# Optimization experiments

Measured on AMD Instinct MI355X. Metric: run time of the kernel, lower is better.

The kernel has to match this reference:

```python
import jax, jax.numpy as jnp
import numpy as np

B, H, W, CIN, C, L = 2, 512, 512, 64, 64, 4
TAU = 1.0


def _conv3x3(x, w):
    # NHWC input, HWIO kernel, SAME zero padding, stride 1 (SignalConv2D corr=True)
    return jax.lax.conv_general_dilated(
        x, w, window_strides=(1, 1), padding='SAME',
        dimension_numbers=('NHWC', 'HWIO', 'NHWC'))


def setup_inputs() -> dict:
    key = jax.random.key(0)
    ks = jax.random.split(key, 10)
    return {
        'x0': jax.random.normal(ks[0], (B, H, W, CIN), jnp.float32),
        'spa_mask': jax.random.uniform(ks[1], (B, H, W, 1), jnp.float32),
        'gumbel_u': jax.random.uniform(ks[2], (1, L, 2, C), jnp.float32),
        'ch_mask': jax.random.uniform(ks[3], (1, L, 2, C), jnp.float32),
        'w0': jax.random.normal(ks[4], (3, 3, CIN, C), jnp.float32) * 0.05,
        'w1': jax.random.normal(ks[5], (3, 3, C, C), jnp.float32) * 0.05,
        'w2': jax.random.normal(ks[6], (3, 3, C, C), jnp.float32) * 0.05,
        'w3': jax.random.normal(ks[7], (3, 3, C, C), jnp.float32) * 0.05,
        'w_collect': jax.random.normal(ks[8], (L * C, C), jnp.float32) * 0.05,
        'b_collect': jnp.zeros((C,), jnp.float32),
    }


def reference(x0, spa_mask, gumbel_u, ch_mask, w0, w1, w2, w3, w_collect, b_collect):
    # Gumbel-softmax channel routing mask over the {dense, sparse} axis (axis=2)
    g = -jnp.log(-jnp.log(jnp.clip(gumbel_u, 1e-10, 1.0)))
    ch = jax.nn.softmax((ch_mask + g) / TAU, axis=2)  # (1, L, 2, C)

    ws = [w0, w1, w2, w3]
    out_feats = []
    fea = x0
    for i in range(L):
        cd = ch[:, i, 0, :][:, None, None, :]  # dense-channel mask  (1,1,1,C)
        cs = ch[:, i, 1, :][:, None, None, :]  # sparse-channel mask (1,1,1,C)
        if i == 0:
            fea = _conv3x3(fea, ws[0])
            fea = fea * cs * spa_mask + fea * cd
        else:
            cdp = ch[:, i - 1, 0, :][:, None, None, :]
            csp = ch[:, i - 1, 1, :][:, None, None, :]
            fea_d = _conv3x3(fea * cdp, ws[i])
            fea_s = _conv3x3(fea * csp, ws[i])
            fea = (fea_d * cs * spa_mask + fea_d * cd
                   + fea_s * cs * spa_mask + fea_s * cd * spa_mask)
        fea = jax.nn.relu(fea)
        out_feats.append(fea)

    cat = jnp.concatenate(out_feats, axis=-1)  # (B, H, W, L*C)
    # 1x1 stride-1 Conv2DTranspose == pointwise linear + bias
    out = jnp.einsum('bhwi,io->bhwo', cat, w_collect) + b_collect
    return out, ch
```

## Files before the change

kernel.cpp:

```cpp
#include <hip/hip_runtime.h>
#include <hip/hip_fp16.h>

#define BB 2
#define HH 512
#define WW 512
#define CC 64
#define PW 514
#define PIMG (514*514)

typedef _Float16 f16;
typedef _Float16 f16x8 __attribute__((ext_vector_type(8)));
typedef _Float16 f16x4 __attribute__((ext_vector_type(4)));
typedef float f32x4 __attribute__((ext_vector_type(4)));

static __device__ __forceinline__ f16x8 zero_f16x8() {
    f16x8 z = {(f16)0,(f16)0,(f16)0,(f16)0,(f16)0,(f16)0,(f16)0,(f16)0};
    return z;
}

static __device__ __forceinline__ f16x8 cvt_pair(f32x4 a, f32x4 b) {
    f16x8 o;
    o[0]=(f16)a[0]; o[1]=(f16)a[1]; o[2]=(f16)a[2]; o[3]=(f16)a[3];
    o[4]=(f16)b[0]; o[5]=(f16)b[1]; o[6]=(f16)b[2]; o[7]=(f16)b[3];
    return o;
}

__global__ void k_prep_ch(const float* __restrict__ gum, const float* __restrict__ chm,
                          float* __restrict__ ws_ch, float* __restrict__ out_ch) {
    int t = threadIdx.x;
    int l = t >> 6, c = t & 63;
    float u0 = gum[(l*2+0)*64+c], u1 = gum[(l*2+1)*64+c];
    u0 = fminf(fmaxf(u0, 1e-10f), 1.0f);
    u1 = fminf(fmaxf(u1, 1e-10f), 1.0f);
    float a0 = chm[(l*2+0)*64+c] - logf(-logf(u0));
    float a1 = chm[(l*2+1)*64+c] - logf(-logf(u1));
    float m = fmaxf(a0, a1);
    float e0 = expf(a0-m), e1 = expf(a1-m);
    float s = e0 + e1;
    float c0 = e0/s, c1 = e1/s;
    ws_ch[(l*2+0)*64+c] = c0;  ws_ch[(l*2+1)*64+c] = c1;
    out_ch[(l*2+0)*64+c] = c0; out_ch[(l*2+1)*64+c] = c1;
}

__global__ void k_pack(const float* __restrict__ w0, const float* __restrict__ w1,
                       const float* __restrict__ w2, const float* __restrict__ w3,
                       const float* __restrict__ wc, const float* __restrict__ ch,
                       f16* __restrict__ bpk0, f16* __restrict__ bpkL, f16* __restrict__ wcpk) {
    int idx = blockIdx.x * 256 + threadIdx.x;
    if (idx < 36864) {
        int j = idx & 7, lane = (idx>>3)&63, nb = (idx>>9)&3, kb = idx>>11;
        int k = kb*32 + (lane>>4)*8 + j;
        int tap = k>>6, ci = k&63;
        int co = nb*16 + (lane&15);
        bpk0[idx] = (f16)w0[(tap*64+ci)*64+co];
    } else if (idx < 36864 + 221184) {
        int i2 = idx - 36864;
        int l = i2 / 73728;
        int r = i2 % 73728;
        int j = r&7, lane=(r>>3)&63, nb=(r>>9)&7, kb=r>>12;
        int k = kb*32 + (lane>>4)*8 + j;
        int tap = k>>6, ci = k&63;
        int copr = nb*16 + (lane&15);
        int co = copr & 63;
        const float* w = (l==0)? w1 : (l==1)? w2 : w3;
        float scale = (copr < 64) ? ch[(l*2+0)*64+ci] : ch[(l*2+1)*64+ci];
        bpkL[i2] = (f16)(w[(tap*64+ci)*64+co] * scale);
    } else if (idx < 36864 + 221184 + 16384) {
        int i3 = idx - (36864 + 221184);
        int j=i3&7, lane=(i3>>3)&63, nb=(i3>>9)&3, kb=(i3>>11)&1, l=i3>>12;
        int k = kb*32 + (lane>>4)*8 + j;
        int n = nb*16 + (lane&15);
        wcpk[i3] = (f16)wc[(l*64+k)*64+n];
    }
}

__global__ void k_guard(f16* __restrict__ buf) {
    int idx = blockIdx.x*256 + threadIdx.x;
    const int TOT = 2*2052*8;
    if (idx >= TOT) return;
    int c8 = idx & 7, g = idx >> 3;
    int b = g / 2052, r = g % 2052;
    int hp, wp;
    if      (r < 514)  { hp = 0;        wp = r; }
    else if (r < 1028) { hp = 513;      wp = r-514; }
    else if (r < 1540) { hp = r-1027;   wp = 0; }
    else               { hp = r-1539;   wp = 513; }
    *(f16x8*)(buf + ((size_t)(b*PW+hp)*PW + wp)*64 + c8*8) = zero_f16x8();
}

template<int MODE>
__global__ __launch_bounds__(256, 2) void k_conv(const void* __restrict__ in_, f16* __restrict__ out,
        const f16* __restrict__ bpk, const float* __restrict__ ch_l,
        const float* __restrict__ spa) {
    constexpr int NBT = (MODE==0) ? 4 : 8;
    constexpr int NF  = (MODE==0) ? 2 : 4;
    __shared__ f16 smem[4*136*64];
    const int wt = blockIdx.x, hb = blockIdx.y, b = blockIdx.z;
    const int h0 = hb*2;
    const int tid = threadIdx.x, lane = tid & 63, wid = tid >> 6;
    const int px0 = wt*128;
    const int sub  = lane & 7;
    const int srel = lane >> 3;
    const int cblk = sub ^ srel;

    const float* inF = (const float*)in_;

    f32x4 v0c[5], v1c[5], v0d[5], v1d[5];
    bool okc[5], okd[5];
    int dstc[5], dstd[5];

    if (MODE == 0) {
        {
            f32x4 v0[9], v1[9];
            bool ok[9];
            int dst[9];
            #pragma unroll
            for (int t = 0; t < 9; ++t) {
                int j = t*4 + wid;
                ok[t] = false;
                if (j < 34) {
                    int r = j / 17, i = j % 17;
                    int s = i*8 + srel;
                    int hin = h0 + r - 1, win = px0 + s - 1;
                    ok[t] = ((unsigned)hin < HH) && ((unsigned)win < WW);
                    dst[t] = r*17408 + i*1024 + lane*16;
                    if (ok[t]) {
                        const f32x4* p = (const f32x4*)(inF + (((size_t)(b*HH + hin)*WW + win)*CC + cblk*8));
                        v0[t] = p[0];
                        v1[t] = p[1];
                    }
                }
            }
            #pragma unroll
            for (int t = 0; t < 9; ++t) {
                if (t*4 + wid < 34) {
                    f16x8 o = ok[t] ? cvt_pair(v0[t], v1[t]) : zero_f16x8();
                    *(f16x8*)((char*)smem + dst[t]) = o;
                }
            }
        }
        __syncthreads();
        #pragma unroll
        for (int t = 0; t < 5; ++t) {
            int i = t*4 + wid;
            okc[t] = false;
            if (i < 17) {
                int s = i*8 + srel;
                int win = px0 + s - 1;
                okc[t] = (unsigned)win < WW;
                dstc[t] = 2*17408 + i*1024 + lane*16;
                if (okc[t]) {
                    const f32x4* p = (const f32x4*)(inF + (((size_t)(b*HH + h0 + 1)*WW + win)*CC + cblk*8));
                    v0c[t] = p[0];
                    v1c[t] = p[1];
                }
            }
        }
        __builtin_amdgcn_sched_barrier(0);
    } else {
        const f16* inH = (const f16*)in_;
        #pragma unroll
        for (int jj = 0; jj < 9; ++jj) {
            int j = jj*4 + wid;
            if (j < 34) {
                int r = j / 17, i = j % 17;
                int s = i*8 + srel;
                const f16* src = inH + ((size_t)(b*PW + h0 + r)*PW + (px0 + s))*64 + cblk*8;
                __builtin_amdgcn_global_load_lds(
                    (const __attribute__((address_space(1))) uint32_t*)src,
                    (__attribute__((address_space(3))) uint32_t*)
                        ((char*)smem + r*17408 + i*1024),
                    16, 0, 0);
            }
        }
        __syncthreads();
        #pragma unroll
        for (int jj = 0; jj < 9; ++jj) {
            int j = 34 + jj*4 + wid;
            if (j < 68) {
                int r = j / 17, i = j % 17;
                int s = i*8 + srel;
                const f16* src = inH + ((size_t)(b*PW + h0 + r)*PW + (px0 + s))*64 + cblk*8;
                __builtin_amdgcn_global_load_lds(
                    (const __attribute__((address_space(1))) uint32_t*)src,
                    (__attribute__((address_space(3))) uint32_t*)
                        ((char*)smem + r*17408 + i*1024),
                    16, 0, 0);
            }
        }
    }

    const int wr = wid >> 1, wn = wid & 1;
    const int lrow = lane & 15, q = lane >> 4;
    const char* smw = (const char*)smem + wr*17408;

    int sb[8][3], po[2][3];
    #pragma unroll
    for (int dxi = 0; dxi < 3; ++dxi) {
        int m7 = (lrow + dxi) & 7;
        po[0][dxi] = ((q)     ^ m7) * 16;
        po[1][dxi] = ((4 + q) ^ m7) * 16;
        #pragma unroll
        for (int mf = 0; mf < 8; ++mf)
            sb[mf][dxi] = (mf*16 + lrow + dxi) * 128;
    }

    f32x4 acc[8][NF];
    #pragma unroll
    for (int i=0;i<8;i++)
        #pragma unroll
        for (int j=0;j<NF;j++) { f32x4 z = {0.f,0.f,0.f,0.f}; acc[i][j] = z; }

    int nbIdx[4];
    nbIdx[0]=wn*2; nbIdx[1]=wn*2+1; nbIdx[2]=wn*2+4; nbIdx[3]=wn*2+5;

    const f16* blane = bpk + (size_t)lane*8;

    f16x8 acur[8], anxt[8], bcur[NF], bnxt[NF];
    #pragma unroll
    for (int nf=0; nf<NF; ++nf)
        bcur[nf] = *reinterpret_cast<const f16x8*>(blane + (size_t)nbIdx[nf]*512);
    #pragma unroll
    for (int mf=0; mf<8; ++mf)
        acur[mf] = *(const f16x8*)(smw + sb[mf][0] + po[0][0]);

    #pragma unroll
    for (int kb = 0; kb < 18; ++kb) {
        if (kb == 5) {
            if (MODE == 0) {
                #pragma unroll
                for (int t = 0; t < 5; ++t) {
                    if (t*4 + wid < 17) {
                        f16x8 o = okc[t] ? cvt_pair(v0c[t], v1c[t]) : zero_f16x8();
                        *(f16x8*)((char*)smem + dstc[t]) = o;
                    }
                }
                #pragma unroll
                for (int t = 0; t < 5; ++t) {
                    int i = t*4 + wid;
                    okd[t] = false;
                    if (i < 17) {
                        int s = i*8 + srel;
                        int hin = h0 + 2, win = px0 + s - 1;
                        okd[t] = ((unsigned)hin < HH) && ((unsigned)win < WW);
                        dstd[t] = 3*17408 + i*1024 + lane*16;
                        if (okd[t]) {
                            const f32x4* p = (const f32x4*)(inF + (((size_t)(b*HH + hin)*WW + win)*CC + cblk*8));
                            v0d[t] = p[0];
                            v1d[t] = p[1];
                        }
                    }
                }
                __builtin_amdgcn_sched_barrier(0);
            }
            __syncthreads();
        }
        if (MODE == 0 && kb == 11) {
            #pragma unroll
            for (int t = 0; t < 5; ++t) {
                if (t*4 + wid < 17) {
                    f16x8 o = okd[t] ? cvt_pair(v0d[t], v1d[t]) : zero_f16x8();
                    *(f16x8*)((char*)smem + dstd[t]) = o;
                }
            }
            __syncthreads();
        }
        if (kb < 17) {
            const int kn = kb + 1;
            const int rn = kn/6, dxin = (kn%6)/2, halfn = kn & 1;
            #pragma unroll
            for (int nf=0; nf<NF; ++nf)
                bnxt[nf] = *reinterpret_cast<const f16x8*>(blane + (size_t)(kn*NBT + nbIdx[nf])*512);
            #pragma unroll
            for (int mf=0; mf<8; ++mf)
                anxt[mf] = *(const f16x8*)(smw + rn*17408 + sb[mf][dxin] + po[halfn][dxin]);
        }
        __builtin_amdgcn_s_setprio(1);
        #pragma unroll
        for (int nf=0; nf<NF; ++nf) {
            #pragma unroll
            for (int mf=0; mf<8; ++mf)
                acc[mf][nf] = __builtin_amdgcn_mfma_f32_16x16x32_f16(acur[mf], bcur[nf], acc[mf][nf], 0,0,0);
        }
        __builtin_amdgcn_s_setprio(0);
        #pragma unroll
        for (int nf=0; nf<NF; ++nf) bcur[nf] = bnxt[nf];
        #pragma unroll
        for (int mf=0; mf<8; ++mf) acur[mf] = anxt[mf];
    }

    const float* cd = ch_l;
    const float* cs = ch_l + 64;
    const int h = h0 + wr;
    const size_t sparow = (size_t)(b*HH + h)*WW;
    const size_t outrow = (size_t)(b*PW + h + 1)*PW + 1;
    #pragma unroll
    for (int mf=0; mf<8; ++mf) {
        const int pixb = mf*16 + q*4;
        f32x4 sp4 = *(const f32x4*)(spa + sparow + px0 + pixb);
        float sp[4] = {sp4[0], sp4[1], sp4[2], sp4[3]};
        #pragma unroll
        for (int nf2=0; nf2<2; ++nf2) {
            int co = wn*32 + nf2*16 + lrow;
            float vcd = cd[co], vcs = cs[co];
            #pragma unroll
            for (int r=0; r<4; ++r) {
                float v;
                if (MODE==0) v = acc[mf][nf2][r] * (vcs*sp[r] + vcd);
                else         v = acc[mf][nf2][r] * (vcs*sp[r] + vcd) + acc[mf][nf2+2][r] * sp[r];
                v = fmaxf(v, 0.f);
                out[(outrow + px0 + pixb + r)*64 + co] = (f16)v;
            }
        }
    }
}

__global__ __launch_bounds__(256) void k_collect_all(
        const f16* __restrict__ f0, const f16* __restrict__ f1,
        const f16* __restrict__ f2, const f16* __restrict__ f3,
        const f16* __restrict__ wcpk, const float* __restrict__ bias,
        float* __restrict__ out) {
    const int wt = blockIdx.x, h = blockIdx.y, b = blockIdx.z;
    const int tid = threadIdx.x;
    const int lane = tid & 63, wid = tid >> 6;
    const int lrow = lane & 15, lk = (lane>>4)*8;
    const size_t inrow  = (size_t)(b*PW + h + 1)*PW + 1;
    const size_t outrow = (size_t)(b*HH + h)*WW;
    const int px0 = wt*256 + wid*64;

    const f16* feas[4] = {f0, f1, f2, f3};

    f32x4 acc[4][4];
    #pragma unroll
    for (int i=0;i<4;i++)
        #pragma unroll
        for (int j=0;j<4;j++) { f32x4 z = {0.f,0.f,0.f,0.f}; acc[i][j] = z; }

    f16x8 a_cur[4], a_nxt[4];
    #pragma unroll
    for (int mf=0; mf<4; ++mf)
        a_cur[mf] = *reinterpret_cast<const f16x8*>(f0 + (inrow + px0 + mf*16 + lrow)*64 + lk);

    #pragma unroll
    for (int kb=0; kb<8; ++kb) {
        if (kb < 7) {
            const f16* fl = feas[(kb+1)>>1];
            #pragma unroll
            for (int mf=0; mf<4; ++mf)
                a_nxt[mf] = *reinterpret_cast<const f16x8*>(fl + (inrow + px0 + mf*16 + lrow)*64 + ((kb+1)&1)*32 + lk);
        }
        #pragma unroll
        for (int nf=0; nf<4; ++nf) {
            f16x8 bb = *reinterpret_cast<const f16x8*>(wcpk + ((size_t)(kb*4 + nf)*64 + lane)*8);
            #pragma unroll
            for (int mf=0; mf<4; ++mf)
                acc[mf][nf] = __builtin_amdgcn_mfma_f32_16x16x32_f16(bb, a_cur[mf], acc[mf][nf], 0,0,0);
        }
        #pragma unroll
        for (int mf=0; mf<4; ++mf) a_cur[mf] = a_nxt[mf];
    }
    const int q = lane >> 4;
    #pragma unroll
    for (int mf=0; mf<4; ++mf) {
        const int pix = px0 + mf*16 + lrow;
        float* orow = out + (outrow + pix)*CC;
        #pragma unroll
        for (int nf=0; nf<4; ++nf) {
            const int co0 = nf*16 + q*4;
            f32x4 b4 = *(const f32x4*)(bias + co0);
            *(f32x4*)(orow + co0) = acc[mf][nf] + b4;
        }
    }
}

template<bool FIRST>
__global__ __launch_bounds__(256) void k_collect(const f16* __restrict__ fea,
        const f16* __restrict__ wcpk_l, const float* __restrict__ bias,
        float* __restrict__ out) {
    const int wt = blockIdx.x, h = blockIdx.y, b = blockIdx.z;
    const int tid = threadIdx.x;
    const int lane = tid & 63, wid = tid >> 6;
    const int lrow = lane & 15, lk = (lane>>4)*8;
    const size_t inrow  = (size_t)(b*PW + h + 1)*PW + 1;
    const size_t outrow = (size_t)(b*HH + h)*WW;
    const int px0 = wt*64 + wid*16;

    f32x4 acc[4];
    #pragma unroll
    for (int j=0;j<4;j++) { f32x4 z = {0.f,0.f,0.f,0.f}; acc[j] = z; }

    #pragma unroll
    for (int kb=0; kb<2; ++kb) {
        f16x8 a = *reinterpret_cast<const f16x8*>(fea + (inrow + px0 + lrow)*64 + kb*32 + lk);
        #pragma unroll
        for (int nf=0; nf<4; ++nf) {
            f16x8 bb = *reinterpret_cast<const f16x8*>(wcpk_l + ((size_t)(kb*4 + nf)*64 + lane)*8);
            acc[nf] = __builtin_amdgcn_mfma_f32_16x16x32_f16(bb, a, acc[nf], 0,0,0);
        }
    }
    const int q = lane >> 4;
    const int pix = px0 + lrow;
    float* orow = out + (outrow + pix)*CC;
    #pragma unroll
    for (int nf=0; nf<4; ++nf) {
        const int co0 = nf*16 + q*4;
        f32x4 v = acc[nf];
        #pragma unroll
        for (int r=0;r<4;++r) {
            float x = v[r];
            if (FIRST) x += bias[co0+r];
            else       x += orow[co0+r];
            orow[co0+r] = x;
        }
    }
}

extern "C" void kernel_launch(void* const* d_in, const int* in_sizes, int n_in,
                              void* d_out, int out_size, void* d_ws, size_t ws_size,
                              hipStream_t stream) {
    const float* x0  = (const float*)d_in[0];
    const float* spa = (const float*)d_in[1];
    const float* gum = (const float*)d_in[2];
    const float* chm = (const float*)d_in[3];
    const float* w0  = (const float*)d_in[4];
    const float* w1  = (const float*)d_in[5];
    const float* w2  = (const float*)d_in[6];
    const float* w3  = (const float*)d_in[7];
    const float* wc  = (const float*)d_in[8];
    const float* bias= (const float*)d_in[9];
    float* out = (float*)d_out;

    char* ws = (char*)d_ws;
    const size_t WBASE = (1u<<20);
    const size_t FB = 67699712ull;
    const size_t NEED_A = WBASE + 4*FB;
    const size_t NEED_B = WBASE + 2*FB;
    if (ws_size < NEED_B) return;

    float* ws_ch = (float*)ws;
    f16* bpk0 = (f16*)(ws + 4096);
    f16* bpkL = (f16*)(ws + 4096 + 73728);
    f16* wcpk = (f16*)(ws + 4096 + 73728 + 442368);

    k_prep_ch<<<1, 256, 0, stream>>>(gum, chm, ws_ch, out + 33554432);
    k_pack<<<1072, 256, 0, stream>>>(w0, w1, w2, w3, wc, ws_ch, bpk0, bpkL, wcpk);

    dim3 gcv(4, 256, 2);
    dim3 gca(2, 512, 2);
    dim3 gcf(8, 512, 2);

    if (ws_size >= NEED_A) {
        f16* R0 = (f16*)(ws + WBASE);
        f16* R1 = (f16*)(ws + WBASE + FB);
        f16* R2 = (f16*)(ws + WBASE + 2*FB);
        f16* R3 = (f16*)(ws + WBASE + 3*FB);
        k_guard<<<129, 256, 0, stream>>>(R1);
        k_guard<<<129, 256, 0, stream>>>(R2);
        k_guard<<<129, 256, 0, stream>>>(R3);
        k_conv<0><<<gcv, 256, 0, stream>>>(x0, R1, bpk0,          ws_ch + 0,   spa);
        k_conv<1><<<gcv, 256, 0, stream>>>(R1, R2, bpkL + 0,      ws_ch + 128, spa);
        k_conv<1><<<gcv, 256, 0, stream>>>(R2, R3, bpkL + 73728,  ws_ch + 256, spa);
        k_conv<1><<<gcv, 256, 0, stream>>>(R3, R0, bpkL + 147456, ws_ch + 384, spa);
        k_collect_all<<<gca, 256, 0, stream>>>(R1, R2, R3, R0, wcpk, bias, out);
    } else {
        f16* P0 = (f16*)(ws + WBASE);
        f16* P1 = (f16*)(ws + WBASE + FB);
        k_guard<<<129, 256, 0, stream>>>(P0);
        k_guard<<<129, 256, 0, stream>>>(P1);
        k_conv<0><<<gcv, 256, 0, stream>>>(x0, P1, bpk0,          ws_ch + 0,   spa);
        k_collect<true ><<<gcf, 256, 0, stream>>>(P1, wcpk + 0,     bias, out);
        k_conv<1><<<gcv, 256, 0, stream>>>(P1, P0, bpkL + 0,      ws_ch + 128, spa);
        k_collect<false><<<gcf, 256, 0, stream>>>(P0, wcpk + 4096,  bias, out);
        k_conv<1><<<gcv, 256, 0, stream>>>(P0, P1, bpkL + 73728,  ws_ch + 256, spa);
        k_collect<false><<<gcf, 256, 0, stream>>>(P1, wcpk + 8192,  bias, out);
        k_conv<1><<<gcv, 256, 0, stream>>>(P1, P0, bpkL + 147456, ws_ch + 384, spa);
        k_collect<false><<<gcf, 256, 0, stream>>>(P0, wcpk + 12288, bias, out);
    }
}
```

Baseline: 357.6 us.

## Shrink conv tile to one output row per block to raise occupancy

Each conv block now computes a single output row instead of two. It stages 3 input rows in shared memory instead of 4, and each wave owns 16 output channels instead of a 2x2 row/channel split. Register use drops because there are fewer accumulators and the A-fragment prefetch double buffer is gone, which allows 3 blocks per SM where launch bounds previously allowed 2. The trade-off is that each block reuses its input rows less, since halo rows are loaded by twice as many blocks. LDS A-loads are also no longer prefetched ahead of the MFMAs.

```diff
diff --git a/kernel.cpp b/kernel.cpp
--- a/kernel.cpp
+++ b/kernel.cpp
@@ -6,11 +6,9 @@
 #define WW 512
 #define CC 64
 #define PW 514
-#define PIMG (514*514)
 
 typedef _Float16 f16;
 typedef _Float16 f16x8 __attribute__((ext_vector_type(8)));
-typedef _Float16 f16x4 __attribute__((ext_vector_type(4)));
 typedef float f32x4 __attribute__((ext_vector_type(4)));
 
 static __device__ __forceinline__ f16x8 zero_f16x8() {
@@ -89,14 +87,13 @@
 }
 
 template<int MODE>
-__global__ __launch_bounds__(256, 2) void k_conv(const void* __restrict__ in_, f16* __restrict__ out,
+__global__ __launch_bounds__(256, 3) void k_conv(const void* __restrict__ in_, f16* __restrict__ out,
         const f16* __restrict__ bpk, const float* __restrict__ ch_l,
         const float* __restrict__ spa) {
     constexpr int NBT = (MODE==0) ? 4 : 8;
-    constexpr int NF  = (MODE==0) ? 2 : 4;
-    __shared__ f16 smem[4*136*64];
-    const int wt = blockIdx.x, hb = blockIdx.y, b = blockIdx.z;
-    const int h0 = hb*2;
+    constexpr int NF  = (MODE==0) ? 1 : 2;
+    __shared__ f16 smem[3*136*64];
+    const int wt = blockIdx.x, h = blockIdx.y, b = blockIdx.z;
     const int tid = threadIdx.x, lane = tid & 63, wid = tid >> 6;
     const int px0 = wt*128;
     const int sub  = lane & 7;
@@ -105,9 +102,9 @@
 
     const float* inF = (const float*)in_;
 
-    f32x4 v0c[5], v1c[5], v0d[5], v1d[5];
-    bool okc[5], okd[5];
-    int dstc[5], dstd[5];
+    f32x4 v0c[5], v1c[5];
+    bool okc[5];
+    int dstc[5];
 
     if (MODE == 0) {
         {
@@ -121,7 +118,7 @@
                 if (j < 34) {
                     int r = j / 17, i = j % 17;
                     int s = i*8 + srel;
-                    int hin = h0 + r - 1, win = px0 + s - 1;
+                    int hin = h + r - 1, win = px0 + s - 1;
                     ok[t] = ((unsigned)hin < HH) && ((unsigned)win < WW);
                     dst[t] = r*17408 + i*1024 + lane*16;
                     if (ok[t]) {
@@ -146,11 +143,11 @@
             okc[t] = false;
             if (i < 17) {
                 int s = i*8 + srel;
-                int win = px0 + s - 1;
-                okc[t] = (unsigned)win < WW;
+                int hin = h + 1, win = px0 + s - 1;
+                okc[t] = ((unsigned)hin < HH) && ((unsigned)win < WW);
                 dstc[t] = 2*17408 + i*1024 + lane*16;
                 if (okc[t]) {
-                    const f32x4* p = (const f32x4*)(inF + (((size_t)(b*HH + h0 + 1)*WW + win)*CC + cblk*8));
+                    const f32x4* p = (const f32x4*)(inF + (((size_t)(b*HH + hin)*WW + win)*CC + cblk*8));
                     v0c[t] = p[0];
                     v1c[t] = p[1];
                 }
@@ -165,7 +162,7 @@
             if (j < 34) {
                 int r = j / 17, i = j % 17;
                 int s = i*8 + srel;
-                const f16* src = inH + ((size_t)(b*PW + h0 + r)*PW + (px0 + s))*64 + cblk*8;
+                const f16* src = inH + ((size_t)(b*PW + h + r)*PW + (px0 + s))*64 + cblk*8;
                 __builtin_amdgcn_global_load_lds(
                     (const __attribute__((address_space(1))) uint32_t*)src,
                     (__attribute__((address_space(3))) uint32_t*)
@@ -175,35 +172,33 @@
         }
         __syncthreads();
         #pragma unroll
-        for (int jj = 0; jj < 9; ++jj) {
-            int j = 34 + jj*4 + wid;
-            if (j < 68) {
-                int r = j / 17, i = j % 17;
+        for (int t = 0; t < 5; ++t) {
+            int i = t*4 + wid;
+            if (i < 17) {
                 int s = i*8 + srel;
-                const f16* src = inH + ((size_t)(b*PW + h0 + r)*PW + (px0 + s))*64 + cblk*8;
+                const f16* src = inH + ((size_t)(b*PW + h + 2)*PW + (px0 + s))*64 + cblk*8;
                 __builtin_amdgcn_global_load_lds(
                     (const __attribute__((address_space(1))) uint32_t*)src,
                     (__attribute__((address_space(3))) uint32_t*)
-                        ((char*)smem + r*17408 + i*1024),
+                        ((char*)smem + 2*17408 + i*1024),
                     16, 0, 0);
             }
         }
     }
 
-    const int wr = wid >> 1, wn = wid & 1;
+    const int wn = wid;
     const int lrow = lane & 15, q = lane >> 4;
-    const char* smw = (const char*)smem + wr*17408;
-
-    int sb[8][3], po[2][3];
+
+    int sb0[8], po[2][3];
     #pragma unroll
     for (int dxi = 0; dxi < 3; ++dxi) {
         int m7 = (lrow + dxi) & 7;
         po[0][dxi] = ((q)     ^ m7) * 16;
         po[1][dxi] = ((4 + q) ^ m7) * 16;
-        #pragma unroll
-        for (int mf = 0; mf < 8; ++mf)
-            sb[mf][dxi] = (mf*16 + lrow + dxi) * 128;
-    }
+    }
+    #pragma unroll
+    for (int mf = 0; mf < 8; ++mf)
+        sb0[mf] = (mf*16 + lrow) * 128;
 
     f32x4 acc[8][NF];
     #pragma unroll
@@ -211,22 +206,19 @@
         #pragma unroll
         for (int j=0;j<NF;j++) { f32x4 z = {0.f,0.f,0.f,0.f}; acc[i][j] = z; }
 
-    int nbIdx[4];
-    nbIdx[0]=wn*2; nbIdx[1]=wn*2+1; nbIdx[2]=wn*2+4; nbIdx[3]=wn*2+5;
+    int nbIdx[2];
+    nbIdx[0] = wn; nbIdx[1] = wn + 4;
 
     const f16* blane = bpk + (size_t)lane*8;
 
-    f16x8 acur[8], anxt[8], bcur[NF], bnxt[NF];
+    f16x8 acur[8], bcur[NF], bnxt[NF];
     #pragma unroll
     for (int nf=0; nf<NF; ++nf)
         bcur[nf] = *reinterpret_cast<const f16x8*>(blane + (size_t)nbIdx[nf]*512);
-    #pragma unroll
-    for (int mf=0; mf<8; ++mf)
-        acur[mf] = *(const f16x8*)(smw + sb[mf][0] + po[0][0]);
 
     #pragma unroll
     for (int kb = 0; kb < 18; ++kb) {
-        if (kb == 5) {
+        if (kb == 11) {
             if (MODE == 0) {
                 #pragma unroll
                 for (int t = 0; t < 5; ++t) {
@@ -235,45 +227,18 @@
                         *(f16x8*)((char*)smem + dstc[t]) = o;
                     }
                 }
-                #pragma unroll
-                for (int t = 0; t < 5; ++t) {
-                    int i = t*4 + wid;
-                    okd[t] = false;
-                    if (i < 17) {
-                        int s = i*8 + srel;
-                        int hin = h0 + 2, win = px0 + s - 1;
-                        okd[t] = ((unsigned)hin < HH) && ((unsigned)win < WW);
-                        dstd[t] = 3*17408 + i*1024 + lane*16;
-                        if (okd[t]) {
-                            const f32x4* p = (const f32x4*)(inF + (((size_t)(b*HH + hin)*WW + win)*CC + cblk*8));
-                            v0d[t] = p[0];
-                            v1d[t] = p[1];
-                        }
-                    }
-                }
-                __builtin_amdgcn_sched_barrier(0);
             }
             __syncthreads();
         }
-        if (MODE == 0 && kb == 11) {
-            #pragma unroll
-            for (int t = 0; t < 5; ++t) {
-                if (t*4 + wid < 17) {
-                    f16x8 o = okd[t] ? cvt_pair(v0d[t], v1d[t]) : zero_f16x8();
-                    *(f16x8*)((char*)smem + dstd[t]) = o;
-                }
-            }
-            __syncthreads();
-        }
+        const int rn = kb/6, dxi = (kb%6)/2, half = kb & 1;
+        #pragma unroll
+        for (int mf=0; mf<8; ++mf)
+            acur[mf] = *(const f16x8*)((const char*)smem + rn*17408 + sb0[mf] + dxi*128 + po[half][dxi]);
         if (kb < 17) {
             const int kn = kb + 1;
-            const int rn = kn/6, dxin = (kn%6)/2, halfn = kn & 1;
             #pragma unroll
             for (int nf=0; nf<NF; ++nf)
                 bnxt[nf] = *reinterpret_cast<const f16x8*>(blane + (size_t)(kn*NBT + nbIdx[nf])*512);
-            #pragma unroll
-            for (int mf=0; mf<8; ++mf)
-                anxt[mf] = *(const f16x8*)(smw + rn*17408 + sb[mf][dxin] + po[halfn][dxin]);
         }
         __builtin_amdgcn_s_setprio(1);
         #pragma unroll
@@ -285,32 +250,26 @@
         __builtin_amdgcn_s_setprio(0);
         #pragma unroll
         for (int nf=0; nf<NF; ++nf) bcur[nf] = bnxt[nf];
-        #pragma unroll
-        for (int mf=0; mf<8; ++mf) acur[mf] = anxt[mf];
     }
 
     const float* cd = ch_l;
     const float* cs = ch_l + 64;
-    const int h = h0 + wr;
     const size_t sparow = (size_t)(b*HH + h)*WW;
     const size_t outrow = (size_t)(b*PW + h + 1)*PW + 1;
+    const int co = wn*16 + lrow;
+    const float vcd = cd[co], vcs = cs[co];
     #pragma unroll
     for (int mf=0; mf<8; ++mf) {
         const int pixb = mf*16 + q*4;
         f32x4 sp4 = *(const f32x4*)(spa + sparow + px0 + pixb);
-        float sp[4] = {sp4[0], sp4[1], sp4[2], sp4[3]};
-        #pragma unroll
-        for (int nf2=0; nf2<2; ++nf2) {
-            int co = wn*32 + nf2*16 + lrow;
-            float vcd = cd[co], vcs = cs[co];
-            #pragma unroll
-            for (int r=0; r<4; ++r) {
-                float v;
-                if (MODE==0) v = acc[mf][nf2][r] * (vcs*sp[r] + vcd);
-                else         v = acc[mf][nf2][r] * (vcs*sp[r] + vcd) + acc[mf][nf2+2][r] * sp[r];
-                v = fmaxf(v, 0.f);
-                out[(outrow + px0 + pixb + r)*64 + co] = (f16)v;
-            }
+        #pragma unroll
+        for (int r=0; r<4; ++r) {
+            float sp = sp4[r];
+            float v;
+            if (MODE==0) v = acc[mf][0][r] * (vcs*sp + vcd);
+            else         v = acc[mf][0][r] * (vcs*sp + vcd) + acc[mf][1][r] * sp;
+            v = fmaxf(v, 0.f);
+            out[(outrow + px0 + pixb + r)*64 + co] = (f16)v;
         }
     }
 }
@@ -445,7 +404,7 @@
     k_prep_ch<<<1, 256, 0, stream>>>(gum, chm, ws_ch, out + 33554432);
     k_pack<<<1072, 256, 0, stream>>>(w0, w1, w2, w3, wc, ws_ch, bpk0, bpkL, wcpk);
 
-    dim3 gcv(4, 256, 2);
+    dim3 gcv(4, 512, 2);
     dim3 gca(2, 512, 2);
     dim3 gcf(8, 512, 2);
 
```

New measurement: 364.0 us. No clear change (+1.8%).
